# Kernel tuning notes

Measured on AMD Instinct MI355X. Metric: run time of the kernel, lower is better.

The kernel has to match this reference:

```python
import jax, jax.numpy as jnp
import numpy as np

B, L, D, A = 64, 512, 512, 512  # batch, seq_len, word_embed_size, alignment_size


def setup_inputs() -> dict:
    key = jax.random.key(0)
    k1, k2, k3 = jax.random.split(key, 3)
    premises = jax.random.normal(k1, (B, L, D), dtype=jnp.float32)
    hypotheses = jax.random.normal(k2, (B, L, D), dtype=jnp.float32)
    W_F = jax.random.uniform(k3, (D, A), dtype=jnp.float32, minval=-1.0, maxval=1.0)
    return {"premises": premises, "hypotheses": hypotheses, "W_F": W_F}


def reference(premises, hypotheses, W_F):
    # tanh-projected cross attention (decomposable-attention align step)
    F_p = jnp.tanh(jnp.einsum('bpd,da->bpa', premises, W_F))    # [B, Lp, A]
    F_h = jnp.tanh(jnp.einsum('bhd,da->bha', hypotheses, W_F))  # [B, Lh, A]
    eijs = jnp.einsum('bpa,bha->bph', F_p, F_h)                 # [B, Lp, Lh] (unscaled)
    attn = jax.nn.softmax(eijs, axis=-1)                        # softmax over hypothesis axis
    betas = jnp.einsum('bph,bhd->bpd', attn, hypotheses)        # [B, Lp, D]
    alphas = jnp.einsum('bph,bpd->bhd', attn, premises)         # [B, Lh, D] (transpose(attn) @ P)
    return betas, alphas
```

## Files before the change

### kernel.cpp

```cpp
#include <hip/hip_runtime.h>
#include <hip/hip_fp16.h>


#define NB 64
#define NL 512
#define ND 512
#define BATCH_ELEMS (512 * 512)
#define TOT_ELEMS   ((size_t)NB * NL * ND)

typedef _Float16 h8 __attribute__((ext_vector_type(8)));
typedef float f4 __attribute__((ext_vector_type(4)));

__device__ __forceinline__ int swz(int row, int chunk) {
    return (row << 5) + ((chunk ^ (((row >> 1) ^ (row >> 4)) & 3)) << 3);
}

__device__ __forceinline__ void gld16(const _Float16* g, _Float16* l) {
    __builtin_amdgcn_global_load_lds(
        (const __attribute__((address_space(1))) void*)g,
        (__attribute__((address_space(3))) void*)l, 16, 0, 0);
}

__device__ __forceinline__ float fast_tanh(float x) {
    float e = __expf(2.0f * x);
    return 1.0f - 2.0f / (e + 1.0f);
}

__global__ __launch_bounds__(256) void conv16_kernel(
    const float* __restrict__ P, const float* __restrict__ H,
    _Float16* __restrict__ X16)
{
    const int z = blockIdx.z;
    const float* src = z ? H : P;
    _Float16* dst = X16 + (size_t)z * TOT_ELEMS;
    size_t i = ((size_t)blockIdx.x * 256 + threadIdx.x) * 8;
    float4 v0 = ((const float4*)(src + i))[0];
    float4 v1 = ((const float4*)(src + i))[1];
    h8 o;
    o[0] = (_Float16)v0.x; o[1] = (_Float16)v0.y;
    o[2] = (_Float16)v0.z; o[3] = (_Float16)v0.w;
    o[4] = (_Float16)v1.x; o[5] = (_Float16)v1.y;
    o[6] = (_Float16)v1.z; o[7] = (_Float16)v1.w;
    *(h8*)(dst + i) = o;
}

template <bool WITH_LO>
__global__ __launch_bounds__(256) void transpose_f16_kernel(
    const float* __restrict__ src, _Float16* __restrict__ dstH,
    _Float16* __restrict__ dstL)
{
    __shared__ float tile[64 * 68];
    const size_t base = (size_t)blockIdx.z * BATCH_ELEMS;
    const int r0 = blockIdx.y * 64, c0 = blockIdx.x * 64;
    const int t = threadIdx.x;
    {
        int r = t >> 2, cq = (t & 3) * 16;
        const float* sp = src + base + (size_t)(r0 + r) * 512 + c0 + cq;
        *(float4*)&tile[r * 68 + cq]      = ((const float4*)sp)[0];
        *(float4*)&tile[r * 68 + cq + 4]  = ((const float4*)sp)[1];
        *(float4*)&tile[r * 68 + cq + 8]  = ((const float4*)sp)[2];
        *(float4*)&tile[r * 68 + cq + 12] = ((const float4*)sp)[3];
    }
    __syncthreads();
    {
        int c = t >> 2, rq = (t & 3) * 16;
        _Float16 hv[16], lv[16];
#pragma unroll
        for (int j = 0; j < 16; ++j) {
            float v = tile[(rq + j) * 68 + c];
            hv[j] = (_Float16)v;
            if (WITH_LO) lv[j] = (_Float16)(v - (float)hv[j]);
        }
        _Float16* dp = dstH + base + (size_t)(c0 + c) * 512 + r0 + rq;
        *(h8*)dp = *(h8*)&hv[0];
        *(h8*)(dp + 8) = *(h8*)&hv[8];
        if (WITH_LO) {
            _Float16* dl = dstL + base + (size_t)(c0 + c) * 512 + r0 + rq;
            *(h8*)dl = *(h8*)&lv[0];
            *(h8*)(dl + 8) = *(h8*)&lv[8];
        }
    }
}

__global__ __launch_bounds__(256) void transpose_hp_kernel(
    const float* __restrict__ H, const float* __restrict__ P,
    _Float16* __restrict__ HT, _Float16* __restrict__ PT)
{
    __shared__ float tile[64 * 68];
    const int z = blockIdx.z;
    const float* src = (z < NB) ? H : P;
    _Float16* dst = (z < NB) ? HT : PT;
    const size_t base = (size_t)(z < NB ? z : z - NB) * BATCH_ELEMS;
    const int r0 = blockIdx.y * 64, c0 = blockIdx.x * 64;
    const int t = threadIdx.x;
    {
        int r = t >> 2, cq = (t & 3) * 16;
        const float* sp = src + base + (size_t)(r0 + r) * 512 + c0 + cq;
        *(float4*)&tile[r * 68 + cq]      = ((const float4*)sp)[0];
        *(float4*)&tile[r * 68 + cq + 4]  = ((const float4*)sp)[1];
        *(float4*)&tile[r * 68 + cq + 8]  = ((const float4*)sp)[2];
        *(float4*)&tile[r * 68 + cq + 12] = ((const float4*)sp)[3];
    }
    __syncthreads();
    {
        int c = t >> 2, rq = (t & 3) * 16;
        _Float16 hv[16];
#pragma unroll
        for (int j = 0; j < 16; ++j) hv[j] = (_Float16)tile[(rq + j) * 68 + c];
        _Float16* dp = dst + base + (size_t)(c0 + c) * 512 + r0 + rq;
        *(h8*)dp = *(h8*)&hv[0];
        *(h8*)(dp + 8) = *(h8*)&hv[8];
    }
}

__global__ __launch_bounds__(256) void proj_tanh_kernel(
    const _Float16* __restrict__ X16,
    const _Float16* __restrict__ WTH, const _Float16* __restrict__ WTL,
    _Float16* __restrict__ Fout)
{
    __shared__ __align__(16) _Float16 AsH[2][128 * 32];
    __shared__ __align__(16) _Float16 BsH[2][128 * 32], BsL[2][128 * 32];

    const int z = blockIdx.z;
    const _Float16* X = X16 + (size_t)z * TOT_ELEMS;
    _Float16* F = Fout + (size_t)z * TOT_ELEMS;
    const int r0 = blockIdx.x * 128;
    const int n0 = blockIdx.y * 128;

    const int t = threadIdx.x;
    const int lane = t & 63, w4 = t >> 6;
    const int q = lane >> 4, c = lane & 15;
    const int wm = w4 >> 1, wn = w4 & 1;

    f4 acc[4][4] = {};

    const int lr = w4 * 16 + (lane >> 2);
    const int sb = ((lr >> 1) ^ (lr >> 4)) & 3;
    const int ch = ((lane & 3) ^ sb) * 8;
    const _Float16* sA0 = X + (size_t)(r0 + lr) * 512 + ch;
    const _Float16* sA1 = sA0 + (size_t)64 * 512;
    const _Float16* sH0 = WTH + (size_t)(n0 + lr) * 512 + ch;
    const _Float16* sH1 = sH0 + (size_t)64 * 512;
    const _Float16* sL0 = WTL + (size_t)(n0 + lr) * 512 + ch;
    const _Float16* sL1 = sL0 + (size_t)64 * 512;
    const int d0 = (w4 * 16) * 32, d1 = (64 + w4 * 16) * 32;

    auto STAGE = [&](int pp, int k0) {
        gld16(sA0 + k0, &AsH[pp][d0]);
        gld16(sA1 + k0, &AsH[pp][d1]);
        gld16(sH0 + k0, &BsH[pp][d0]);
        gld16(sH1 + k0, &BsH[pp][d1]);
        gld16(sL0 + k0, &BsL[pp][d0]);
        gld16(sL1 + k0, &BsL[pp][d1]);
    };

    STAGE(0, 0);
    __syncthreads();

    for (int ks = 0; ks < 16; ++ks) {
        const int pp = ks & 1;
        if (ks + 1 < 16) STAGE(pp ^ 1, (ks + 1) << 5);

        h8 aH[4], bH[4], bL[4];
#pragma unroll
        for (int mi = 0; mi < 4; ++mi)
            aH[mi] = *(const h8*)&AsH[pp][swz(wm * 64 + mi * 16 + c, q)];
#pragma unroll
        for (int ni = 0; ni < 4; ++ni) {
            bH[ni] = *(const h8*)&BsH[pp][swz(wn * 64 + ni * 16 + c, q)];
            bL[ni] = *(const h8*)&BsL[pp][swz(wn * 64 + ni * 16 + c, q)];
        }
#pragma unroll
        for (int mi = 0; mi < 4; ++mi)
#pragma unroll
            for (int ni = 0; ni < 4; ++ni) {
                acc[mi][ni] = __builtin_amdgcn_mfma_f32_16x16x32_f16(aH[mi], bH[ni], acc[mi][ni], 0, 0, 0);
                acc[mi][ni] = __builtin_amdgcn_mfma_f32_16x16x32_f16(aH[mi], bL[ni], acc[mi][ni], 0, 0, 0);
            }
        __syncthreads();
    }

#pragma unroll
    for (int mi = 0; mi < 4; ++mi)
#pragma unroll
        for (int ni = 0; ni < 4; ++ni) {
            int col = n0 + wn * 64 + ni * 16 + c;
            int rowb = r0 + wm * 64 + mi * 16 + q * 4;
#pragma unroll
            for (int r = 0; r < 4; ++r)
                F[(size_t)(rowb + r) * 512 + col] = (_Float16)fast_tanh(acc[mi][ni][r]);
        }
}

__global__ __launch_bounds__(256) void score_softmax_kernel(
    const _Float16* __restrict__ Fbase, _Float16* __restrict__ attn)
{
    __shared__ __align__(16) _Float16 As[2][64 * 32];
    __shared__ __align__(16) _Float16 Bs[2][512 * 32];
    __shared__ float redM[4 * 64], redS[4 * 64];

    const _Float16* Fp = Fbase;
    const _Float16* Fh = Fbase + TOT_ELEMS;
    const int b = blockIdx.y;
    const int p0 = blockIdx.x * 64;
    const size_t fb = (size_t)b * BATCH_ELEMS;

    const int t = threadIdx.x, lane = t & 63, w = t >> 6;
    const int q = lane >> 4, c = lane & 15;

    f4 acc[4][8] = {};

    const int lr = w * 16 + (lane >> 2);
    const int sb = ((lr >> 1) ^ (lr >> 4)) & 3;
    const int ch = ((lane & 3) ^ sb) * 8;
    const _Float16* sA  = Fp + fb + (size_t)(p0 + lr) * 512 + ch;
    const _Float16* sB0 = Fh + fb + (size_t)lr * 512 + ch;
    const int dA = (w * 16) * 32;

    auto STAGE = [&](int pp, int k0) {
        gld16(sA + k0, &As[pp][dA]);
#pragma unroll
        for (int i = 0; i < 8; ++i)
            gld16(sB0 + (size_t)i * 64 * 512 + k0, &Bs[pp][(i * 64 + w * 16) * 32]);
    };

    STAGE(0, 0);
    __syncthreads();

    for (int ks = 0; ks < 16; ++ks) {
        const int pp = ks & 1;
        if (ks + 1 < 16) STAGE(pp ^ 1, (ks + 1) << 5);

        h8 a[4], bb[8];
#pragma unroll
        for (int mt = 0; mt < 4; ++mt) a[mt] = *(const h8*)&As[pp][swz(mt * 16 + c, q)];
#pragma unroll
        for (int nt = 0; nt < 8; ++nt) bb[nt] = *(const h8*)&Bs[pp][swz(w * 128 + nt * 16 + c, q)];
#pragma unroll
        for (int mt = 0; mt < 4; ++mt)
#pragma unroll
            for (int nt = 0; nt < 8; ++nt)
                acc[mt][nt] = __builtin_amdgcn_mfma_f32_16x16x32_f16(a[mt], bb[nt], acc[mt][nt], 0, 0, 0);
        __syncthreads();
    }

    float rmax[4][4];
#pragma unroll
    for (int mt = 0; mt < 4; ++mt)
#pragma unroll
        for (int r = 0; r < 4; ++r) {
            float m = acc[mt][0][r];
#pragma unroll
            for (int nt = 1; nt < 8; ++nt) m = fmaxf(m, acc[mt][nt][r]);
            rmax[mt][r] = m;
        }
#pragma unroll
    for (int s = 1; s < 16; s <<= 1)
#pragma unroll
        for (int mt = 0; mt < 4; ++mt)
#pragma unroll
            for (int r = 0; r < 4; ++r)
                rmax[mt][r] = fmaxf(rmax[mt][r], __shfl_xor(rmax[mt][r], s, 64));
    if (c == 0)
#pragma unroll
        for (int mt = 0; mt < 4; ++mt)
#pragma unroll
            for (int r = 0; r < 4; ++r)
                redM[w * 64 + mt * 16 + q * 4 + r] = rmax[mt][r];
    __syncthreads();

    float gmax[4][4];
#pragma unroll
    for (int mt = 0; mt < 4; ++mt)
#pragma unroll
        for (int r = 0; r < 4; ++r) {
            int row = mt * 16 + q * 4 + r;
            float m = redM[row];
#pragma unroll
            for (int w4i = 1; w4i < 4; ++w4i) m = fmaxf(m, redM[w4i * 64 + row]);
            gmax[mt][r] = m;
        }

    float rsum[4][4] = {};
#pragma unroll
    for (int mt = 0; mt < 4; ++mt)
#pragma unroll
        for (int nt = 0; nt < 8; ++nt)
#pragma unroll
            for (int r = 0; r < 4; ++r) {
                float e = __expf(acc[mt][nt][r] - gmax[mt][r]);
                acc[mt][nt][r] = e;
                rsum[mt][r] += e;
            }
#pragma unroll
    for (int s = 1; s < 16; s <<= 1)
#pragma unroll
        for (int mt = 0; mt < 4; ++mt)
#pragma unroll
            for (int r = 0; r < 4; ++r)
                rsum[mt][r] += __shfl_xor(rsum[mt][r], s, 64);
    if (c == 0)
#pragma unroll
        for (int mt = 0; mt < 4; ++mt)
#pragma unroll
            for (int r = 0; r < 4; ++r)
                redS[w * 64 + mt * 16 + q * 4 + r] = rsum[mt][r];
    __syncthreads();

    float inv[4][4];
#pragma unroll
    for (int mt = 0; mt < 4; ++mt)
#pragma unroll
        for (int r = 0; r < 4; ++r) {
            int row = mt * 16 + q * 4 + r;
            float s = redS[row] + redS[64 + row] + redS[128 + row] + redS[192 + row];
            inv[mt][r] = 1.0f / s;
        }

#pragma unroll
    for (int mt = 0; mt < 4; ++mt)
#pragma unroll
        for (int nt = 0; nt < 8; ++nt) {
            int col = w * 128 + nt * 16 + c;
#pragma unroll
            for (int r = 0; r < 4; ++r) {
                int row = p0 + mt * 16 + q * 4 + r;
                attn[fb + (size_t)row * 512 + col] = (_Float16)(acc[mt][nt][r] * inv[mt][r]);
            }
        }
}

__global__ __launch_bounds__(256) void out_gemm_kernel(
    const _Float16* __restrict__ Amat, const _Float16* __restrict__ HT,
    const _Float16* __restrict__ PT, float* __restrict__ out)
{
    __shared__ __align__(16) _Float16 As[2][128 * 32];
    __shared__ __align__(16) _Float16 Bs[2][128 * 32];

    const int zz = blockIdx.z;
    const bool transA = zz >= NB;
    const int b = transA ? zz - NB : zz;
    const _Float16* BT = transA ? PT : HT;
    float* Cout = transA ? out + TOT_ELEMS : out;

    const int bn = blockIdx.x * 128, bm = blockIdx.y * 128;
    const size_t base = (size_t)b * BATCH_ELEMS;

    const int t = threadIdx.x, lane = t & 63, w4 = t >> 6;
    const int q = lane >> 4, c = lane & 15;
    const int wm = w4 >> 1, wn = w4 & 1;

    f4 acc[4][4] = {};

    const int lr = w4 * 16 + (lane >> 2);
    const int sb = ((lr >> 1) ^ (lr >> 4)) & 3;
    const int ch = ((lane & 3) ^ sb) * 8;
    const _Float16* sA0 = Amat + base + (size_t)(bm + lr) * 512 + ch;
    const _Float16* sA1 = sA0 + (size_t)64 * 512;
    const _Float16* sB0 = BT + base + (size_t)(bn + lr) * 512 + ch;
    const _Float16* sB1 = sB0 + (size_t)64 * 512;
    const int d0 = (w4 * 16) * 32, d1 = (64 + w4 * 16) * 32;

    const int kk = t >> 3, m0 = (t & 7) * 16;
    const _Float16* apg_t = Amat + base + (size_t)kk * 512 + bm + m0;
    h8 a0, a1;

    auto STAGE_B = [&](int pp, int k0) {
        gld16(sB0 + k0, &Bs[pp][d0]);
        gld16(sB1 + k0, &Bs[pp][d1]);
    };
    auto STAGE_A_DIRECT = [&](int pp, int k0) {
        gld16(sA0 + k0, &As[pp][d0]);
        gld16(sA1 + k0, &As[pp][d1]);
    };
    auto LOAD_A_T = [&](int k0) {
        a0 = ((const h8*)(apg_t + (size_t)k0 * 512))[0];
        a1 = ((const h8*)(apg_t + (size_t)k0 * 512))[1];
    };
    auto STAGE_A_T = [&](int pp) {
#pragma unroll
        for (int j = 0; j < 8; ++j) {
            As[pp][swz(m0 + j, kk >> 3) + (kk & 7)]     = a0[j];
            As[pp][swz(m0 + 8 + j, kk >> 3) + (kk & 7)] = a1[j];
        }
    };

    STAGE_B(0, 0);
    if (!transA) {
        STAGE_A_DIRECT(0, 0);
    } else {
        LOAD_A_T(0);
        STAGE_A_T(0);
    }
    __syncthreads();

    for (int ks = 0; ks < 16; ++ks) {
        const int pp = ks & 1;
        const bool more = (ks + 1) < 16;
        const int k0n = (ks + 1) << 5;
        if (more) {
            STAGE_B(pp ^ 1, k0n);
            if (!transA) STAGE_A_DIRECT(pp ^ 1, k0n);
            else LOAD_A_T(k0n);
        }

        h8 a[4], bb[4];
#pragma unroll
        for (int mi = 0; mi < 4; ++mi) a[mi] = *(const h8*)&As[pp][swz(wm * 64 + mi * 16 + c, q)];
#pragma unroll
        for (int ni = 0; ni < 4; ++ni) bb[ni] = *(const h8*)&Bs[pp][swz(wn * 64 + ni * 16 + c, q)];
#pragma unroll
        for (int mi = 0; mi < 4; ++mi)
#pragma unroll
            for (int ni = 0; ni < 4; ++ni)
                acc[mi][ni] = __builtin_amdgcn_mfma_f32_16x16x32_f16(a[mi], bb[ni], acc[mi][ni], 0, 0, 0);
        if (more && transA) STAGE_A_T(pp ^ 1);
        __syncthreads();
    }

#pragma unroll
    for (int mi = 0; mi < 4; ++mi)
#pragma unroll
        for (int ni = 0; ni < 4; ++ni) {
            int col = bn + wn * 64 + ni * 16 + c;
            int rowb = bm + wm * 64 + mi * 16 + q * 4;
#pragma unroll
            for (int r = 0; r < 4; ++r)
                Cout[base + (size_t)(rowb + r) * 512 + col] = acc[mi][ni][r];
        }
}

extern "C" void kernel_launch(void* const* d_in, const int* in_sizes, int n_in,
                              void* d_out, int out_size, void* d_ws, size_t ws_size,
                              hipStream_t stream) {
    const float* P = (const float*)d_in[0];
    const float* H = (const float*)d_in[1];
    const float* W = (const float*)d_in[2];
    float* out = (float*)d_out;

    _Float16* ws16 = (_Float16*)d_ws;
    _Float16* F    = ws16;
    _Float16* PT   = ws16;
    _Float16* HT   = ws16 + TOT_ELEMS;
    _Float16* attn = ws16 + 2 * TOT_ELEMS;
    _Float16* WTH  = attn;
    _Float16* WTL  = attn + BATCH_ELEMS;
    _Float16* X16  = (_Float16*)d_out;

    conv16_kernel<<<dim3(8192, 1, 2), 256, 0, stream>>>(P, H, X16);
    transpose_f16_kernel<true><<<dim3(8, 8, 1), 256, 0, stream>>>(W, WTH, WTL);
    proj_tanh_kernel<<<dim3(256, 4, 2), 256, 0, stream>>>(X16, WTH, WTL, F);
    score_softmax_kernel<<<dim3(8, NB), 256, 0, stream>>>(F, attn);
    transpose_hp_kernel<<<dim3(8, 8, 2 * NB), 256, 0, stream>>>(H, P, HT, PT);
    out_gemm_kernel<<<dim3(4, 4, 2 * NB), 256, 0, stream>>>(attn, HT, PT, out);
}
```

Baseline: 503.9 us.

## Load GEMM B operands directly to registers and transpose from fp16 copies

In the projection and output GEMMs, the B operand is now read from global memory straight into MFMA register fragments and prefetched one k-step ahead, instead of being staged through LDS. This drops the B shared buffers and lets the kernels declare a 3-block occupancy hint. The H/P transpose now reads the existing fp16 copies (X16) rather than fp32 inputs, which halves its read traffic, and uses an XOR-swizzled fp16 LDS tile. The trade-off is less coalesced 16-byte global reads for B and more register pressure. The transpose also relies on X16 still holding valid data when it runs, since that buffer lives in the output array.

```diff
diff --git a/kernel.cpp b/kernel.cpp
--- a/kernel.cpp
+++ b/kernel.cpp
@@ -82,44 +82,44 @@
     }
 }
 
-__global__ __launch_bounds__(256) void transpose_hp_kernel(
-    const float* __restrict__ H, const float* __restrict__ P,
-    _Float16* __restrict__ HT, _Float16* __restrict__ PT)
-{
-    __shared__ float tile[64 * 68];
-    const int z = blockIdx.z;
-    const float* src = (z < NB) ? H : P;
-    _Float16* dst = (z < NB) ? HT : PT;
-    const size_t base = (size_t)(z < NB ? z : z - NB) * BATCH_ELEMS;
+__global__ __launch_bounds__(256) void transpose_hp16_kernel(
+    const _Float16* __restrict__ X16, _Float16* __restrict__ dstbase)
+{
+    __shared__ __align__(16) _Float16 tile[64 * 64];
+    const size_t base = (size_t)blockIdx.z * BATCH_ELEMS;
     const int r0 = blockIdx.y * 64, c0 = blockIdx.x * 64;
     const int t = threadIdx.x;
     {
         int r = t >> 2, cq = (t & 3) * 16;
-        const float* sp = src + base + (size_t)(r0 + r) * 512 + c0 + cq;
-        *(float4*)&tile[r * 68 + cq]      = ((const float4*)sp)[0];
-        *(float4*)&tile[r * 68 + cq + 4]  = ((const float4*)sp)[1];
-        *(float4*)&tile[r * 68 + cq + 8]  = ((const float4*)sp)[2];
-        *(float4*)&tile[r * 68 + cq + 12] = ((const float4*)sp)[3];
+        const _Float16* sp = X16 + base + (size_t)(r0 + r) * 512 + c0 + cq;
+        h8 v0 = ((const h8*)sp)[0];
+        h8 v1 = ((const h8*)sp)[1];
+        int f = ((r >> 1) ^ (r >> 4)) & 7;
+        *(h8*)&tile[r * 64 + (((cq >> 3) ^ f) << 3)]       = v0;
+        *(h8*)&tile[r * 64 + ((((cq >> 3) + 1) ^ f) << 3)] = v1;
     }
     __syncthreads();
     {
         int c = t >> 2, rq = (t & 3) * 16;
         _Float16 hv[16];
 #pragma unroll
-        for (int j = 0; j < 16; ++j) hv[j] = (_Float16)tile[(rq + j) * 68 + c];
-        _Float16* dp = dst + base + (size_t)(c0 + c) * 512 + r0 + rq;
+        for (int j = 0; j < 16; ++j) {
+            int row = rq + j;
+            int f = ((row >> 1) ^ (row >> 4)) & 7;
+            hv[j] = tile[row * 64 + (((c >> 3) ^ f) << 3) + (c & 7)];
+        }
+        _Float16* dp = dstbase + base + (size_t)(c0 + c) * 512 + r0 + rq;
         *(h8*)dp = *(h8*)&hv[0];
         *(h8*)(dp + 8) = *(h8*)&hv[8];
     }
 }
 
-__global__ __launch_bounds__(256) void proj_tanh_kernel(
+__global__ __launch_bounds__(256, 3) void proj_tanh_kernel(
     const _Float16* __restrict__ X16,
     const _Float16* __restrict__ WTH, const _Float16* __restrict__ WTL,
     _Float16* __restrict__ Fout)
 {
     __shared__ __align__(16) _Float16 AsH[2][128 * 32];
-    __shared__ __align__(16) _Float16 BsH[2][128 * 32], BsL[2][128 * 32];
 
     const int z = blockIdx.z;
     const _Float16* X = X16 + (size_t)z * TOT_ELEMS;
@@ -139,45 +139,57 @@
     const int ch = ((lane & 3) ^ sb) * 8;
     const _Float16* sA0 = X + (size_t)(r0 + lr) * 512 + ch;
     const _Float16* sA1 = sA0 + (size_t)64 * 512;
-    const _Float16* sH0 = WTH + (size_t)(n0 + lr) * 512 + ch;
-    const _Float16* sH1 = sH0 + (size_t)64 * 512;
-    const _Float16* sL0 = WTL + (size_t)(n0 + lr) * 512 + ch;
-    const _Float16* sL1 = sL0 + (size_t)64 * 512;
     const int d0 = (w4 * 16) * 32, d1 = (64 + w4 * 16) * 32;
 
-    auto STAGE = [&](int pp, int k0) {
+    const _Float16* bhg = WTH + (size_t)(n0 + wn * 64 + c) * 512 + q * 8;
+    const _Float16* blg = WTL + (size_t)(n0 + wn * 64 + c) * 512 + q * 8;
+
+    auto STAGE_A = [&](int pp, int k0) {
         gld16(sA0 + k0, &AsH[pp][d0]);
         gld16(sA1 + k0, &AsH[pp][d1]);
-        gld16(sH0 + k0, &BsH[pp][d0]);
-        gld16(sH1 + k0, &BsH[pp][d1]);
-        gld16(sL0 + k0, &BsL[pp][d0]);
-        gld16(sL1 + k0, &BsL[pp][d1]);
     };
 
-    STAGE(0, 0);
-    __syncthreads();
-
+    h8 bHc[4], bLc[4];
+#pragma unroll
+    for (int ni = 0; ni < 4; ++ni) {
+        bHc[ni] = *(const h8*)(bhg + (size_t)ni * 16 * 512);
+        bLc[ni] = *(const h8*)(blg + (size_t)ni * 16 * 512);
+    }
+    STAGE_A(0, 0);
+    __syncthreads();
+
+#pragma unroll
     for (int ks = 0; ks < 16; ++ks) {
         const int pp = ks & 1;
-        if (ks + 1 < 16) STAGE(pp ^ 1, (ks + 1) << 5);
-
-        h8 aH[4], bH[4], bL[4];
+        const bool more = (ks + 1) < 16;
+        const int k0n = (ks + 1) << 5;
+        if (more) STAGE_A(pp ^ 1, k0n);
+
+        h8 bHn[4], bLn[4];
+        if (more) {
+#pragma unroll
+            for (int ni = 0; ni < 4; ++ni) {
+                bHn[ni] = *(const h8*)(bhg + (size_t)ni * 16 * 512 + k0n);
+                bLn[ni] = *(const h8*)(blg + (size_t)ni * 16 * 512 + k0n);
+            }
+        }
+
+        h8 aH[4];
 #pragma unroll
         for (int mi = 0; mi < 4; ++mi)
             aH[mi] = *(const h8*)&AsH[pp][swz(wm * 64 + mi * 16 + c, q)];
 #pragma unroll
-        for (int ni = 0; ni < 4; ++ni) {
-            bH[ni] = *(const h8*)&BsH[pp][swz(wn * 64 + ni * 16 + c, q)];
-            bL[ni] = *(const h8*)&BsL[pp][swz(wn * 64 + ni * 16 + c, q)];
-        }
-#pragma unroll
         for (int mi = 0; mi < 4; ++mi)
 #pragma unroll
             for (int ni = 0; ni < 4; ++ni) {
-                acc[mi][ni] = __builtin_amdgcn_mfma_f32_16x16x32_f16(aH[mi], bH[ni], acc[mi][ni], 0, 0, 0);
-                acc[mi][ni] = __builtin_amdgcn_mfma_f32_16x16x32_f16(aH[mi], bL[ni], acc[mi][ni], 0, 0, 0);
+                acc[mi][ni] = __builtin_amdgcn_mfma_f32_16x16x32_f16(aH[mi], bHc[ni], acc[mi][ni], 0, 0, 0);
+                acc[mi][ni] = __builtin_amdgcn_mfma_f32_16x16x32_f16(aH[mi], bLc[ni], acc[mi][ni], 0, 0, 0);
             }
         __syncthreads();
+        if (more) {
+#pragma unroll
+            for (int ni = 0; ni < 4; ++ni) { bHc[ni] = bHn[ni]; bLc[ni] = bLn[ni]; }
+        }
     }
 
 #pragma unroll
@@ -330,12 +342,11 @@
         }
 }
 
-__global__ __launch_bounds__(256) void out_gemm_kernel(
+__global__ __launch_bounds__(256, 3) void out_gemm_kernel(
     const _Float16* __restrict__ Amat, const _Float16* __restrict__ HT,
     const _Float16* __restrict__ PT, float* __restrict__ out)
 {
     __shared__ __align__(16) _Float16 As[2][128 * 32];
-    __shared__ __align__(16) _Float16 Bs[2][128 * 32];
 
     const int zz = blockIdx.z;
     const bool transA = zz >= NB;
@@ -357,18 +368,14 @@
     const int ch = ((lane & 3) ^ sb) * 8;
     const _Float16* sA0 = Amat + base + (size_t)(bm + lr) * 512 + ch;
     const _Float16* sA1 = sA0 + (size_t)64 * 512;
-    const _Float16* sB0 = BT + base + (size_t)(bn + lr) * 512 + ch;
-    const _Float16* sB1 = sB0 + (size_t)64 * 512;
     const int d0 = (w4 * 16) * 32, d1 = (64 + w4 * 16) * 32;
 
     const int kk = t >> 3, m0 = (t & 7) * 16;
     const _Float16* apg_t = Amat + base + (size_t)kk * 512 + bm + m0;
     h8 a0, a1;
 
-    auto STAGE_B = [&](int pp, int k0) {
-        gld16(sB0 + k0, &Bs[pp][d0]);
-        gld16(sB1 + k0, &Bs[pp][d1]);
-    };
+    const _Float16* bfg = BT + base + (size_t)(bn + wn * 64 + c) * 512 + q * 8;
+
     auto STAGE_A_DIRECT = [&](int pp, int k0) {
         gld16(sA0 + k0, &As[pp][d0]);
         gld16(sA1 + k0, &As[pp][d1]);
@@ -385,7 +392,10 @@
         }
     };
 
-    STAGE_B(0, 0);
+    h8 bbc[4];
+#pragma unroll
+    for (int ni = 0; ni < 4; ++ni)
+        bbc[ni] = *(const h8*)(bfg + (size_t)ni * 16 * 512);
     if (!transA) {
         STAGE_A_DIRECT(0, 0);
     } else {
@@ -394,28 +404,36 @@
     }
     __syncthreads();
 
+#pragma unroll
     for (int ks = 0; ks < 16; ++ks) {
         const int pp = ks & 1;
         const bool more = (ks + 1) < 16;
         const int k0n = (ks + 1) << 5;
         if (more) {
-            STAGE_B(pp ^ 1, k0n);
             if (!transA) STAGE_A_DIRECT(pp ^ 1, k0n);
             else LOAD_A_T(k0n);
         }
-
-        h8 a[4], bb[4];
+        h8 bbn[4];
+        if (more) {
+#pragma unroll
+            for (int ni = 0; ni < 4; ++ni)
+                bbn[ni] = *(const h8*)(bfg + (size_t)ni * 16 * 512 + k0n);
+        }
+
+        h8 a[4];
 #pragma unroll
         for (int mi = 0; mi < 4; ++mi) a[mi] = *(const h8*)&As[pp][swz(wm * 64 + mi * 16 + c, q)];
 #pragma unroll
-        for (int ni = 0; ni < 4; ++ni) bb[ni] = *(const h8*)&Bs[pp][swz(wn * 64 + ni * 16 + c, q)];
-#pragma unroll
         for (int mi = 0; mi < 4; ++mi)
 #pragma unroll
             for (int ni = 0; ni < 4; ++ni)
-                acc[mi][ni] = __builtin_amdgcn_mfma_f32_16x16x32_f16(a[mi], bb[ni], acc[mi][ni], 0, 0, 0);
+                acc[mi][ni] = __builtin_amdgcn_mfma_f32_16x16x32_f16(a[mi], bbc[ni], acc[mi][ni], 0, 0, 0);
         if (more && transA) STAGE_A_T(pp ^ 1);
         __syncthreads();
+        if (more) {
+#pragma unroll
+            for (int ni = 0; ni < 4; ++ni) bbc[ni] = bbn[ni];
+        }
     }
 
 #pragma unroll
@@ -451,6 +469,6 @@
     transpose_f16_kernel<true><<<dim3(8, 8, 1), 256, 0, stream>>>(W, WTH, WTL);
     proj_tanh_kernel<<<dim3(256, 4, 2), 256, 0, stream>>>(X16, WTH, WTL, F);
     score_softmax_kernel<<<dim3(8, NB), 256, 0, stream>>>(F, attn);
-    transpose_hp_kernel<<<dim3(8, 8, 2 * NB), 256, 0, stream>>>(H, P, HT, PT);
+    transpose_hp16_kernel<<<dim3(8, 8, 2 * NB), 256, 0, stream>>>(X16, ws16);
     out_gemm_kernel<<<dim3(4, 4, 2 * NB), 256, 0, stream>>>(attn, HT, PT, out);
 }
```

Result: slower. 535.8 us (+6.3%).

## Fuse betas GEMM into score-softmax kernel and drop P transpose

Applied to the files above, without the earlier changes.

The betas product (attn @ H) moves into the score/softmax kernel, so each block multiplies its freshly written attn rows by a transposed half-precision H read straight from global memory. H is now transposed from the already-converted fp16 copy instead of from fp32. The alphas GEMM reads P in fp32, converts it to fp16 and stages it into LDS transposed, so the separate P transpose pass is gone. This cuts kernel launches and the extra transpose traffic, but the fused kernel does more work per block at a low grid size (8x64), and its B operand is loaded without LDS staging.

```diff
diff --git a/kernel.cpp b/kernel.cpp
--- a/kernel.cpp
+++ b/kernel.cpp
@@ -82,32 +82,33 @@
     }
 }
 
-__global__ __launch_bounds__(256) void transpose_hp_kernel(
-    const float* __restrict__ H, const float* __restrict__ P,
-    _Float16* __restrict__ HT, _Float16* __restrict__ PT)
-{
-    __shared__ float tile[64 * 68];
-    const int z = blockIdx.z;
-    const float* src = (z < NB) ? H : P;
-    _Float16* dst = (z < NB) ? HT : PT;
-    const size_t base = (size_t)(z < NB ? z : z - NB) * BATCH_ELEMS;
+__global__ __launch_bounds__(256) void transpose_h16_kernel(
+    const _Float16* __restrict__ Xh, _Float16* __restrict__ HT)
+{
+    __shared__ __align__(16) _Float16 tile[64 * 64];
+    const size_t base = (size_t)blockIdx.z * BATCH_ELEMS;
     const int r0 = blockIdx.y * 64, c0 = blockIdx.x * 64;
     const int t = threadIdx.x;
     {
         int r = t >> 2, cq = (t & 3) * 16;
-        const float* sp = src + base + (size_t)(r0 + r) * 512 + c0 + cq;
-        *(float4*)&tile[r * 68 + cq]      = ((const float4*)sp)[0];
-        *(float4*)&tile[r * 68 + cq + 4]  = ((const float4*)sp)[1];
-        *(float4*)&tile[r * 68 + cq + 8]  = ((const float4*)sp)[2];
-        *(float4*)&tile[r * 68 + cq + 12] = ((const float4*)sp)[3];
+        const _Float16* sp = Xh + base + (size_t)(r0 + r) * 512 + c0 + cq;
+        h8 v0 = ((const h8*)sp)[0];
+        h8 v1 = ((const h8*)sp)[1];
+        int f = ((r >> 1) ^ (r >> 4)) & 7;
+        *(h8*)&tile[r * 64 + (((cq >> 3) ^ f) << 3)]       = v0;
+        *(h8*)&tile[r * 64 + ((((cq >> 3) + 1) ^ f) << 3)] = v1;
     }
     __syncthreads();
     {
         int c = t >> 2, rq = (t & 3) * 16;
         _Float16 hv[16];
 #pragma unroll
-        for (int j = 0; j < 16; ++j) hv[j] = (_Float16)tile[(rq + j) * 68 + c];
-        _Float16* dp = dst + base + (size_t)(c0 + c) * 512 + r0 + rq;
+        for (int j = 0; j < 16; ++j) {
+            int row = rq + j;
+            int f = ((row >> 1) ^ (row >> 4)) & 7;
+            hv[j] = tile[row * 64 + (((c >> 3) ^ f) << 3) + (c & 7)];
+        }
+        _Float16* dp = HT + base + (size_t)(c0 + c) * 512 + r0 + rq;
         *(h8*)dp = *(h8*)&hv[0];
         *(h8*)(dp + 8) = *(h8*)&hv[8];
     }
@@ -192,8 +193,9 @@
         }
 }
 
-__global__ __launch_bounds__(256) void score_softmax_kernel(
-    const _Float16* __restrict__ Fbase, _Float16* __restrict__ attn)
+__global__ __launch_bounds__(256) void score_softmax_beta_kernel(
+    const _Float16* __restrict__ Fbase, const _Float16* __restrict__ HT,
+    _Float16* __restrict__ attn, float* __restrict__ outB)
 {
     __shared__ __align__(16) _Float16 As[2][64 * 32];
     __shared__ __align__(16) _Float16 Bs[2][512 * 32];
@@ -328,21 +330,56 @@
                 attn[fb + (size_t)row * 512 + col] = (_Float16)(acc[mt][nt][r] * inv[mt][r]);
             }
         }
-}
-
-__global__ __launch_bounds__(256) void out_gemm_kernel(
-    const _Float16* __restrict__ Amat, const _Float16* __restrict__ HT,
-    const _Float16* __restrict__ PT, float* __restrict__ out)
+    __syncthreads();
+
+    f4 bacc[4][8] = {};
+    const _Float16* sA2 = attn + fb + (size_t)(p0 + lr) * 512 + ch;
+    const _Float16* bhg = HT + fb + (size_t)(w * 128 + c) * 512 + q * 8;
+
+    gld16(sA2, &As[0][dA]);
+    __syncthreads();
+
+    for (int ks = 0; ks < 16; ++ks) {
+        const int pp = ks & 1;
+        const int k0 = ks << 5;
+        if (ks + 1 < 16) gld16(sA2 + ((ks + 1) << 5), &As[pp ^ 1][dA]);
+
+        h8 bb2[8];
+#pragma unroll
+        for (int nt = 0; nt < 8; ++nt)
+            bb2[nt] = *(const h8*)(bhg + (size_t)nt * 16 * 512 + k0);
+        h8 a2[4];
+#pragma unroll
+        for (int mt = 0; mt < 4; ++mt) a2[mt] = *(const h8*)&As[pp][swz(mt * 16 + c, q)];
+#pragma unroll
+        for (int mt = 0; mt < 4; ++mt)
+#pragma unroll
+            for (int nt = 0; nt < 8; ++nt)
+                bacc[mt][nt] = __builtin_amdgcn_mfma_f32_16x16x32_f16(a2[mt], bb2[nt], bacc[mt][nt], 0, 0, 0);
+        __syncthreads();
+    }
+
+#pragma unroll
+    for (int mt = 0; mt < 4; ++mt)
+#pragma unroll
+        for (int nt = 0; nt < 8; ++nt) {
+            int col = w * 128 + nt * 16 + c;
+#pragma unroll
+            for (int r = 0; r < 4; ++r) {
+                int row = p0 + mt * 16 + q * 4 + r;
+                outB[fb + (size_t)row * 512 + col] = bacc[mt][nt][r];
+            }
+        }
+}
+
+__global__ __launch_bounds__(256) void alphas_gemm_kernel(
+    const _Float16* __restrict__ attn, const float* __restrict__ P,
+    float* __restrict__ outA)
 {
     __shared__ __align__(16) _Float16 As[2][128 * 32];
     __shared__ __align__(16) _Float16 Bs[2][128 * 32];
 
-    const int zz = blockIdx.z;
-    const bool transA = zz >= NB;
-    const int b = transA ? zz - NB : zz;
-    const _Float16* BT = transA ? PT : HT;
-    float* Cout = transA ? out + TOT_ELEMS : out;
-
+    const int b = blockIdx.z;
     const int bn = blockIdx.x * 128, bm = blockIdx.y * 128;
     const size_t base = (size_t)b * BATCH_ELEMS;
 
@@ -352,57 +389,40 @@
 
     f4 acc[4][4] = {};
 
-    const int lr = w4 * 16 + (lane >> 2);
-    const int sb = ((lr >> 1) ^ (lr >> 4)) & 3;
-    const int ch = ((lane & 3) ^ sb) * 8;
-    const _Float16* sA0 = Amat + base + (size_t)(bm + lr) * 512 + ch;
-    const _Float16* sA1 = sA0 + (size_t)64 * 512;
-    const _Float16* sB0 = BT + base + (size_t)(bn + lr) * 512 + ch;
-    const _Float16* sB1 = sB0 + (size_t)64 * 512;
-    const int d0 = (w4 * 16) * 32, d1 = (64 + w4 * 16) * 32;
-
     const int kk = t >> 3, m0 = (t & 7) * 16;
-    const _Float16* apg_t = Amat + base + (size_t)kk * 512 + bm + m0;
+    const _Float16* apg = attn + base + (size_t)kk * 512 + bm + m0;
+    const float*    bpg = P    + base + (size_t)kk * 512 + bn + m0;
+
     h8 a0, a1;
-
-    auto STAGE_B = [&](int pp, int k0) {
-        gld16(sB0 + k0, &Bs[pp][d0]);
-        gld16(sB1 + k0, &Bs[pp][d1]);
+    float bv[16];
+
+    auto LOAD = [&](int k0) {
+        a0 = ((const h8*)(apg + (size_t)k0 * 512))[0];
+        a1 = ((const h8*)(apg + (size_t)k0 * 512))[1];
+        const float* bp = bpg + (size_t)k0 * 512;
+        *(float4*)&bv[0]  = ((const float4*)bp)[0];
+        *(float4*)&bv[4]  = ((const float4*)bp)[1];
+        *(float4*)&bv[8]  = ((const float4*)bp)[2];
+        *(float4*)&bv[12] = ((const float4*)bp)[3];
     };
-    auto STAGE_A_DIRECT = [&](int pp, int k0) {
-        gld16(sA0 + k0, &As[pp][d0]);
-        gld16(sA1 + k0, &As[pp][d1]);
-    };
-    auto LOAD_A_T = [&](int k0) {
-        a0 = ((const h8*)(apg_t + (size_t)k0 * 512))[0];
-        a1 = ((const h8*)(apg_t + (size_t)k0 * 512))[1];
-    };
-    auto STAGE_A_T = [&](int pp) {
+    auto STAGE = [&](int pp) {
 #pragma unroll
         for (int j = 0; j < 8; ++j) {
             As[pp][swz(m0 + j, kk >> 3) + (kk & 7)]     = a0[j];
             As[pp][swz(m0 + 8 + j, kk >> 3) + (kk & 7)] = a1[j];
+            Bs[pp][swz(m0 + j, kk >> 3) + (kk & 7)]     = (_Float16)bv[j];
+            Bs[pp][swz(m0 + 8 + j, kk >> 3) + (kk & 7)] = (_Float16)bv[8 + j];
         }
     };
 
-    STAGE_B(0, 0);
-    if (!transA) {
-        STAGE_A_DIRECT(0, 0);
-    } else {
-        LOAD_A_T(0);
-        STAGE_A_T(0);
-    }
-    __syncthreads();
-
-    for (int ks = 0; ks < 16; ++ks) {
-        const int pp = ks & 1;
-        const bool more = (ks + 1) < 16;
-        const int k0n = (ks + 1) << 5;
-        if (more) {
-            STAGE_B(pp ^ 1, k0n);
-            if (!transA) STAGE_A_DIRECT(pp ^ 1, k0n);
-            else LOAD_A_T(k0n);
-        }
+    LOAD(0);
+    STAGE(0);
+
+    int pp = 0;
+    for (int k0 = 0; k0 < 512; k0 += 32) {
+        __syncthreads();
+        const bool more = (k0 + 32) < 512;
+        if (more) LOAD(k0 + 32);
 
         h8 a[4], bb[4];
 #pragma unroll
@@ -414,8 +434,8 @@
 #pragma unroll
             for (int ni = 0; ni < 4; ++ni)
                 acc[mi][ni] = __builtin_amdgcn_mfma_f32_16x16x32_f16(a[mi], bb[ni], acc[mi][ni], 0, 0, 0);
-        if (more && transA) STAGE_A_T(pp ^ 1);
-        __syncthreads();
+        if (more) STAGE(pp ^ 1);
+        pp ^= 1;
     }
 
 #pragma unroll
@@ -426,7 +446,7 @@
             int rowb = bm + wm * 64 + mi * 16 + q * 4;
 #pragma unroll
             for (int r = 0; r < 4; ++r)
-                Cout[base + (size_t)(rowb + r) * 512 + col] = acc[mi][ni][r];
+                outA[base + (size_t)(rowb + r) * 512 + col] = acc[mi][ni][r];
         }
 }
 
@@ -440,17 +460,16 @@
 
     _Float16* ws16 = (_Float16*)d_ws;
     _Float16* F    = ws16;
-    _Float16* PT   = ws16;
-    _Float16* HT   = ws16 + TOT_ELEMS;
     _Float16* attn = ws16 + 2 * TOT_ELEMS;
     _Float16* WTH  = attn;
     _Float16* WTL  = attn + BATCH_ELEMS;
     _Float16* X16  = (_Float16*)d_out;
+    _Float16* HT   = X16 + 2 * TOT_ELEMS;
 
     conv16_kernel<<<dim3(8192, 1, 2), 256, 0, stream>>>(P, H, X16);
     transpose_f16_kernel<true><<<dim3(8, 8, 1), 256, 0, stream>>>(W, WTH, WTL);
+    transpose_h16_kernel<<<dim3(8, 8, NB), 256, 0, stream>>>(X16 + TOT_ELEMS, HT);
     proj_tanh_kernel<<<dim3(256, 4, 2), 256, 0, stream>>>(X16, WTH, WTL, F);
-    score_softmax_kernel<<<dim3(8, NB), 256, 0, stream>>>(F, attn);
-    transpose_hp_kernel<<<dim3(8, 8, 2 * NB), 256, 0, stream>>>(H, P, HT, PT);
-    out_gemm_kernel<<<dim3(4, 4, 2 * NB), 256, 0, stream>>>(attn, HT, PT, out);
-}
+    score_softmax_beta_kernel<<<dim3(8, NB), 256, 0, stream>>>(F, HT, attn, out);
+    alphas_gemm_kernel<<<dim3(4, 4, NB), 256, 0, stream>>>(attn, P, out + TOT_ELEMS);
+}
```

New measurement: 504.0 us. No clear change (+0.0%).
